# Optimization experiments

Measured on AMD Instinct MI355X. Metric: run time of the kernel, lower is better.

The kernel has to match this reference:

```python
import jax, jax.numpy as jnp
import numpy as np

D = 1024
H = 16
HD = D // H  # 64
FF = 4 * D
EPS = 1e-5


def _xavier(key, shape):
    fan_in, fan_out = shape[1], shape[0]
    limit = float(np.sqrt(6.0 / (fan_in + fan_out)))
    return jax.random.uniform(key, shape, jnp.float32, -limit, limit)


def setup_inputs() -> dict:
    key = jax.random.key(0)
    ks = jax.random.split(key, 8)
    x = jax.random.normal(ks[0], (2, 2048, D), jnp.float32)
    return {
        "x": x,
        "w_qkv": _xavier(ks[1], (3 * D, D)),
        "b_qkv": jnp.zeros((3 * D,), jnp.float32),
        "w_out": _xavier(ks[2], (D, D)),
        "b_out": jnp.zeros((D,), jnp.float32),
        "w1": _xavier(ks[3], (FF, D)),
        "b1": jnp.zeros((FF,), jnp.float32),
        "w2": _xavier(ks[4], (D, FF)),
        "b2": jnp.zeros((D,), jnp.float32),
        "ln1_g": jnp.ones((D,), jnp.float32),
        "ln1_b": jnp.zeros((D,), jnp.float32),
        "ln2_g": jnp.ones((D,), jnp.float32),
        "ln2_b": jnp.zeros((D,), jnp.float32),
    }


def _layernorm(x, g, b):
    mu = jnp.mean(x, -1, keepdims=True)
    var = jnp.mean(jnp.square(x - mu), -1, keepdims=True)
    return (x - mu) * jax.lax.rsqrt(var + EPS) * g + b


def reference(x, w_qkv, b_qkv, w_out, b_out, w1, b1, w2, b2,
              ln1_g, ln1_b, ln2_g, ln2_b):
    B, S, _ = x.shape
    # pre-LN attention branch
    h = _layernorm(x, ln1_g, ln1_b)
    qkv = h @ w_qkv.T + b_qkv                      # [B,S,3D]
    qkv = qkv.reshape(B, S, H, 3 * HD).transpose(0, 2, 1, 3)  # [B,H,S,3hd]
    q, k, v = jnp.split(qkv, 3, axis=-1)
    scores = jnp.einsum('bhqd,bhkd->bhqk', q, k) / np.sqrt(HD)
    attn = jax.nn.softmax(scores, axis=-1)
    ctx = jnp.einsum('bhqk,bhkd->bhqd', attn, v)   # [B,H,S,hd]
    ctx = ctx.transpose(0, 2, 1, 3).reshape(B, S, D)
    x = x + (ctx @ w_out.T + b_out)
    # pre-LN MLP branch
    h = _layernorm(x, ln2_g, ln2_b)
    h = jax.nn.relu(h @ w1.T + b1)
    x = x + (h @ w2.T + b2)
    return x
```

## Files before the change

kernel.cpp:

```cpp
#include <hip/hip_runtime.h>
#include <hip/hip_bf16.h>

typedef __attribute__((ext_vector_type(8))) short bf16x8;
typedef __attribute__((ext_vector_type(4))) float f32x4;
typedef __attribute__((ext_vector_type(16))) float f32x16;
typedef __attribute__((ext_vector_type(4))) unsigned short u16x4;
typedef __attribute__((ext_vector_type(4))) unsigned int u32x4;
typedef unsigned short u16;

__device__ __forceinline__ u16 f2bf(float f) {
  unsigned u = __builtin_bit_cast(unsigned, f);
  u += 0x7fffu + ((u >> 16) & 1u);
  return (u16)(u >> 16);
}
__device__ __forceinline__ float bf2f(u16 u) {
  unsigned v = ((unsigned)u) << 16;
  return __builtin_bit_cast(float, v);
}
__device__ __forceinline__ unsigned cvt_pk_bf16(float lo, float hi) {
  unsigned r;
  asm("v_cvt_pk_bf16_f32 %0, %1, %2" : "=v"(r) : "v"(lo), "v"(hi));
  return r;
}
__device__ __forceinline__ float exp2_fast(float x) {
  float r;
  asm("v_exp_f32 %0, %1" : "=v"(r) : "v"(x));
  return r;
}

__device__ __forceinline__ void gl_lds16(const void* g, void* l) {
  __builtin_amdgcn_global_load_lds((const __attribute__((address_space(1))) void*)g,
                                   (__attribute__((address_space(3))) void*)l,
                                   16, 0, 0);
}

__device__ __forceinline__ void bar() {
  asm volatile("" ::: "memory");
  __builtin_amdgcn_s_barrier();
  asm volatile("" ::: "memory");
}

__global__ __launch_bounds__(256) void cvt_all(const float* __restrict__ a,
                                               const float* __restrict__ b,
                                               const float* __restrict__ c,
                                               const float* __restrict__ d,
                                               u16* __restrict__ oa,
                                               u16* __restrict__ ob,
                                               u16* __restrict__ oc,
                                               u16* __restrict__ od) {
  int i = blockIdx.x * 256 + threadIdx.x;
  const int stride = gridDim.x * 256;
  for (; i < 3145728; i += stride) {
    const float* src;
    u16* dst;
    int j;
    if (i < 786432) { src = a; dst = oa; j = i; }
    else if (i < 1048576) { src = b; dst = ob; j = i - 786432; }
    else if (i < 2097152) { src = c; dst = oc; j = i - 1048576; }
    else { src = d; dst = od; j = i - 2097152; }
    float4 v = ((const float4*)src)[j];
    u16x4 o;
    o.x = f2bf(v.x); o.y = f2bf(v.y); o.z = f2bf(v.z); o.w = f2bf(v.w);
    ((u16x4*)dst)[j] = o;
  }
}

__global__ __launch_bounds__(256) void ln_k(const float* __restrict__ x,
                                            const float* __restrict__ g,
                                            const float* __restrict__ b,
                                            u16* __restrict__ out) {
  const int row = blockIdx.x;
  const int t = threadIdx.x;
  const int lane = t & 63, w = t >> 6;
  const float4 v = ((const float4*)(x + (size_t)row * 1024))[t];
  float s = v.x + v.y + v.z + v.w;
  float q = v.x * v.x + v.y * v.y + v.z * v.z + v.w * v.w;
#pragma unroll
  for (int off = 32; off; off >>= 1) {
    s += __shfl_down(s, off);
    q += __shfl_down(q, off);
  }
  __shared__ float red[8];
  if (lane == 0) { red[w] = s; red[4 + w] = q; }
  __syncthreads();
  s = red[0] + red[1] + red[2] + red[3];
  q = red[4] + red[5] + red[6] + red[7];
  const float mu = s * (1.f / 1024.f);
  const float var = q * (1.f / 1024.f) - mu * mu;
  const float rs = rsqrtf(var + 1e-5f);
  const float4 gv = ((const float4*)g)[t];
  const float4 bv = ((const float4*)b)[t];
  u16x4 o;
  o.x = f2bf((v.x - mu) * rs * gv.x + bv.x);
  o.y = f2bf((v.y - mu) * rs * gv.y + bv.y);
  o.z = f2bf((v.z - mu) * rs * gv.z + bv.z);
  o.w = f2bf((v.w - mu) * rs * gv.w + bv.w);
  ((u16x4*)(out + (size_t)row * 1024))[t] = o;
}

template <int BM, int BN, int TH, int WN, int MR, int NR, int EPI>
__global__ __launch_bounds__(TH, 2) void gemm_rot(const u16* __restrict__ A,
                                                  const u16* __restrict__ B,
                                                  const float* __restrict__ bias,
                                                  const float* __restrict__ res,
                                                  void* __restrict__ outp,
                                                  const int N, const int K) {
  constexpr int AELEMS = BM * 32;
  constexpr int BELEMS = BN * 32;
  constexpr int NC = (BM + BN) * 4 / TH;
  static_assert((BM * 4) % TH == 0 && ((BM + BN) * 4) % TH == 0, "");
  __shared__ u16 lds[3][AELEMS + BELEMS];
  const int t = threadIdx.x;
  const int lane = t & 63, w = t >> 6;
  const int wm = w / WN, wn = w % WN;
  const int l15 = lane & 15, lhi = lane >> 4;
  const int nbx = gridDim.x;
  const int nwg = nbx * gridDim.y;
  const int orig = blockIdx.y * nbx + blockIdx.x;
  const int cpx = nwg >> 3;
  const int lid = (orig & 7) * cpx + (orig >> 3);
  const long bm = (long)(lid / nbx) * BM, bn = (long)(lid % nbx) * BN;
  const u16* Ab = A + bm * K;
  const u16* Bb = B + bn * K;
  const int nk = K >> 5;

#define STAGE(kt_, bufi)                                                      \
  do {                                                                        \
    const long kk_ = (long)(kt_) << 5;                                        \
    _Pragma("unroll")                                                         \
    for (int j = 0; j < NC; ++j) {                                            \
      const int sj = j * TH + t;                                              \
      const u16* src_;                                                        \
      if ((j + 1) * TH <= BM * 4) {                                           \
        src_ = Ab + (size_t)(sj >> 2) * K + kk_ + ((sj & 3) ^ ((sj >> 3) & 3)) * 8; \
      } else {                                                                \
        const int sb_ = sj - BM * 4;                                          \
        src_ = Bb + (size_t)(sb_ >> 2) * K + kk_ + ((sb_ & 3) ^ ((sb_ >> 3) & 3)) * 8; \
      }                                                                       \
      gl_lds16(src_, &lds[bufi][(size_t)(j * TH + w * 64) * 8]);              \
    }                                                                         \
  } while (0)

  f32x4 acc[MR][NR] = {};
  STAGE(0, 0);
  STAGE(1, 1);
  STAGE(2, 2);
  for (int i = 0; i < nk; ++i) {
    if (i + 2 < nk) {
      if constexpr (NC == 4) asm volatile("s_waitcnt vmcnt(8)" ::: "memory");
      else                   asm volatile("s_waitcnt vmcnt(6)" ::: "memory");
    } else if (i + 1 < nk) {
      if constexpr (NC == 4) asm volatile("s_waitcnt vmcnt(4)" ::: "memory");
      else                   asm volatile("s_waitcnt vmcnt(3)" ::: "memory");
    } else {
      asm volatile("s_waitcnt vmcnt(0)" ::: "memory");
    }
    bar();
    const u16* bufA = lds[i % 3];
    const u16* bufB = bufA + AELEMS;
    bf16x8 av[MR], bv[NR];
#pragma unroll
    for (int ii = 0; ii < MR; ++ii) {
      const int R = wm * (MR * 16) + ii * 16 + l15;
      av[ii] = *(const bf16x8*)&bufA[R * 32 + ((lhi ^ ((R >> 1) & 3)) << 3)];
    }
#pragma unroll
    for (int jj = 0; jj < NR; ++jj) {
      const int R = wn * (NR * 16) + jj * 16 + l15;
      bv[jj] = *(const bf16x8*)&bufB[R * 32 + ((lhi ^ ((R >> 1) & 3)) << 3)];
    }
    __builtin_amdgcn_s_setprio(1);
#pragma unroll
    for (int ii = 0; ii < MR; ++ii)
#pragma unroll
      for (int jj = 0; jj < NR; ++jj)
        acc[ii][jj] = __builtin_amdgcn_mfma_f32_16x16x32_bf16(av[ii], bv[jj], acc[ii][jj], 0, 0, 0);
    __builtin_amdgcn_s_setprio(0);
    bar();
    if (i + 3 < nk) STAGE(i + 3, i % 3);
  }
#undef STAGE
#pragma unroll
  for (int jj = 0; jj < NR; ++jj) {
    const long col = bn + wn * (NR * 16) + jj * 16 + l15;
    const float bj = bias[col];
#pragma unroll
    for (int ii = 0; ii < MR; ++ii) {
      const long row0 = bm + wm * (MR * 16) + ii * 16 + lhi * 4;
#pragma unroll
      for (int r = 0; r < 4; ++r) {
        const float v = acc[ii][jj][r] + bj;
        const long idx = (row0 + r) * N + col;
        if constexpr (EPI == 0) {
          ((u16*)outp)[idx] = f2bf(v);
        } else if constexpr (EPI == 1) {
          ((float*)outp)[idx] = v + res[idx];
        } else {
          ((u16*)outp)[idx] = f2bf(v > 0.f ? v : 0.f);
        }
      }
    }
  }
}

__global__ __launch_bounds__(256) void vtrans(const u16* __restrict__ qkv,
                                              u16* __restrict__ vt) {
  const int t = threadIdx.x;
  const int bh = blockIdx.y, b = bh >> 4, h = bh & 15;
  const int kvb = blockIdx.x * 64;
  __shared__ u16 tile[64][72];
  const u16* src = qkv + ((size_t)(b * 2048 + kvb)) * 3072 + h * 192 + 128;
#pragma unroll
  for (int rr = 0; rr < 2; ++rr) {
    const int e = rr * 2048 + t * 8;
    const int kv = e >> 6, d = e & 63;
    *(bf16x8*)&tile[kv][d] = *(const bf16x8*)(src + (size_t)kv * 3072 + d);
  }
  __syncthreads();
#pragma unroll
  for (int rr = 0; rr < 2; ++rr) {
    const int e = rr * 2048 + t * 8;
    const int d = e >> 6, kv = e & 63;
    bf16x8 o;
#pragma unroll
    for (int j = 0; j < 8; ++j) o[j] = (short)tile[kv + j][d];
    *(bf16x8*)(vt + ((size_t)bh * 64 + d) * 2048 + kvb + kv) = o;
  }
}

__global__ __launch_bounds__(256, 4) void attn_k(const u16* __restrict__ qkv,
                                                 const u16* __restrict__ vt,
                                                 u16* __restrict__ part0,
                                                 u16* __restrict__ part1,
                                                 float* __restrict__ ml) {
  __shared__ u16 kt[2][4096];
  __shared__ u16 vtl[2][4096];
  const int t = threadIdx.x;
  const int lane = t & 63, w = t >> 6;
  const int l31 = lane & 31, hl = lane >> 5;
  const int l7 = l31 & 7;
  const int bh = blockIdx.y, b = bh >> 4, h = bh & 15;
  const int qb = blockIdx.x * 128 + w * 32;
  const int sidx = blockIdx.z;
  const int kvbeg = sidx * 1024, kvend = kvbeg + 1024;

  const float qscale = 0.125f * 1.44269504f;
  const u16* qp = qkv + ((size_t)(b * 2048 + qb + l31)) * 3072 + h * 192;
  bf16x8 qf[4];
#pragma unroll
  for (int ds = 0; ds < 4; ++ds) {
    bf16x8 v = *(const bf16x8*)(qp + 16 * ds + 8 * hl);
#pragma unroll
    for (int j = 0; j < 8; ++j) v[j] = (short)f2bf(bf2f((u16)v[j]) * qscale);
    qf[ds] = v;
  }

  const int srow = t >> 3, sgc = t & 7;
  const int sswz = (sgc ^ (srow & 7)) * 8;
  const u16* kg0 = qkv + ((size_t)(b * 2048 + srow)) * 3072 + h * 192 + 64 + sswz;
  const u16* vg0 = vt + (size_t)bh * 64 * 2048 + (size_t)srow * 2048 + sswz;

  f32x16 o0 = {}, o1 = {};
  float m = -1e30f, lsum = 0.f;

#define STAGE(bufi, kv0i)                                              \
  do {                                                                 \
    const u16* ks_ = kg0 + (size_t)(kv0i) * 3072;                      \
    const u16* vs_ = vg0 + (kv0i);                                     \
    gl_lds16(ks_, &kt[bufi][w * 512]);                                 \
    gl_lds16(ks_ + (size_t)32 * 3072, &kt[bufi][2048 + w * 512]);      \
    gl_lds16(vs_, &vtl[bufi][w * 512]);                                \
    gl_lds16(vs_ + (size_t)32 * 2048, &vtl[bufi][2048 + w * 512]);     \
  } while (0)

#define PACK(dst, SA, tl)                                                 \
  do {                                                                    \
    unsigned A0 = cvt_pk_bf16(SA[8 * tl + 0], SA[8 * tl + 1]);            \
    unsigned A1 = cvt_pk_bf16(SA[8 * tl + 2], SA[8 * tl + 3]);            \
    unsigned B0 = cvt_pk_bf16(SA[8 * tl + 4], SA[8 * tl + 5]);            \
    unsigned B1 = cvt_pk_bf16(SA[8 * tl + 6], SA[8 * tl + 7]);            \
    asm volatile("v_permlane32_swap_b32 %0, %1" : "+v"(A0), "+v"(B0));    \
    asm volatile("v_permlane32_swap_b32 %0, %1" : "+v"(A1), "+v"(B1));    \
    u32x4 pv_ = {A0, A1, B0, B1};                                         \
    dst = __builtin_bit_cast(bf16x8, pv_);                                \
  } while (0)

  int buf = 0;
  STAGE(0, kvbeg);
  for (int kv0 = kvbeg; kv0 < kvend; kv0 += 64) {
    if (kv0 + 64 < kvend) {
      STAGE(buf ^ 1, kv0 + 64);
      asm volatile("s_waitcnt vmcnt(4)" ::: "memory");
    } else {
      asm volatile("s_waitcnt vmcnt(0)" ::: "memory");
    }
    bar();
    f32x16 sa0 = {}, sa1 = {};
    __builtin_amdgcn_s_setprio(1);
#pragma unroll
    for (int ds = 0; ds < 4; ++ds) {
      const bf16x8 kf0 = *(const bf16x8*)&kt[buf][l31 * 64 + (((2 * ds + hl) ^ l7) << 3)];
      const bf16x8 kf1 = *(const bf16x8*)&kt[buf][(32 + l31) * 64 + (((2 * ds + hl) ^ l7) << 3)];
      sa0 = __builtin_amdgcn_mfma_f32_32x32x16_bf16(kf0, qf[ds], sa0, 0, 0, 0);
      sa1 = __builtin_amdgcn_mfma_f32_32x32x16_bf16(kf1, qf[ds], sa1, 0, 0, 0);
    }
    __builtin_amdgcn_s_setprio(0);
    float mx[16];
#pragma unroll
    for (int i = 0; i < 16; ++i) mx[i] = fmaxf(sa0[i], sa1[i]);
    const float t0 = fmaxf(fmaxf(mx[0], mx[1]), mx[2]);
    const float t1 = fmaxf(fmaxf(mx[3], mx[4]), mx[5]);
    const float t2 = fmaxf(fmaxf(mx[6], mx[7]), mx[8]);
    const float t3 = fmaxf(fmaxf(mx[9], mx[10]), mx[11]);
    const float t4 = fmaxf(fmaxf(mx[12], mx[13]), mx[14]);
    const float u0 = fmaxf(fmaxf(t0, t1), t2);
    const float u1 = fmaxf(fmaxf(t3, t4), mx[15]);
    float pmax = fmaxf(u0, u1);
    pmax = fmaxf(pmax, __shfl_xor(pmax, 32));
    if (!__all(pmax <= m + 8.f)) {
      const float mn = fmaxf(m, pmax);
      const float sc = exp2_fast(m - mn);
      m = mn;
      lsum *= sc;
      o0 *= sc;
      o1 *= sc;
    }
#pragma unroll
    for (int i = 0; i < 16; ++i) sa0[i] = exp2_fast(sa0[i] - m);
#pragma unroll
    for (int i = 0; i < 16; ++i) sa1[i] = exp2_fast(sa1[i] - m);
    float sm[16];
#pragma unroll
    for (int i = 0; i < 16; ++i) sm[i] = sa0[i] + sa1[i];
#pragma unroll
    for (int st = 8; st; st >>= 1)
#pragma unroll
      for (int i = 0; i < st; ++i) sm[i] += sm[i + st];
    lsum += sm[0] + __shfl_xor(sm[0], 32);
    bf16x8 pf0, pf1, pf2, pf3;
    PACK(pf0, sa0, 0);
    PACK(pf1, sa0, 1);
    PACK(pf2, sa1, 0);
    PACK(pf3, sa1, 1);
    __builtin_amdgcn_s_setprio(1);
#pragma unroll
    for (int t4i = 0; t4i < 4; ++t4i) {
      const bf16x8 vf0 = *(const bf16x8*)&vtl[buf][l31 * 64 + (((2 * t4i + hl) ^ l7) << 3)];
      const bf16x8 vf1 = *(const bf16x8*)&vtl[buf][(32 + l31) * 64 + (((2 * t4i + hl) ^ l7) << 3)];
      const bf16x8 pf = (t4i == 0) ? pf0 : (t4i == 1) ? pf1 : (t4i == 2) ? pf2 : pf3;
      o0 = __builtin_amdgcn_mfma_f32_32x32x16_bf16(vf0, pf, o0, 0, 0, 0);
      o1 = __builtin_amdgcn_mfma_f32_32x32x16_bf16(vf1, pf, o1, 0, 0, 0);
    }
    __builtin_amdgcn_s_setprio(0);
    bar();
    buf ^= 1;
  }
#undef STAGE
#undef PACK
  if (lane < 32) {
    const size_t mi = ((size_t)(sidx * 32 + bh) * 2048 + qb + l31) * 2;
    ml[mi] = m;
    ml[mi + 1] = lsum;
  }
  u16* obase = (sidx == 0) ? part0 : part1;
  u16* ow = ((u16*)kt) + w * 2048;
#pragma unroll
  for (int g2 = 0; g2 < 4; ++g2) {
    uint2 v0, v1;
    v0.x = cvt_pk_bf16(o0[4 * g2 + 0], o0[4 * g2 + 1]);
    v0.y = cvt_pk_bf16(o0[4 * g2 + 2], o0[4 * g2 + 3]);
    v1.x = cvt_pk_bf16(o1[4 * g2 + 0], o1[4 * g2 + 1]);
    v1.y = cvt_pk_bf16(o1[4 * g2 + 2], o1[4 * g2 + 3]);
    *(uint2*)&ow[l31 * 64 + ((g2 ^ l7) << 3) + hl * 4] = v0;
    *(uint2*)&ow[l31 * 64 + (((4 + g2) ^ l7) << 3) + hl * 4] = v1;
  }
#pragma unroll
  for (int p = 0; p < 4; ++p) {
    const int q = 8 * p + (lane >> 3);
    const int gpos = lane & 7;
    const bf16x8 val = *(const bf16x8*)&ow[q * 64 + (gpos << 3)];
    const int gd = gpos ^ (q & 7);
    *(bf16x8*)(obase + ((size_t)(b * 2048 + qb + q)) * 1024 + h * 64 + gd * 8) = val;
  }
}

__global__ __launch_bounds__(256) void attn_merge(const u16* __restrict__ p1,
                                                  const float* __restrict__ ml,
                                                  u16* __restrict__ ctx) {
  const int c = blockIdx.x * 256 + threadIdx.x;
  const int row = c >> 7;
  const int b = row >> 11, q = row & 2047;
  const int h = (c >> 3) & 15;
  const int bh = b * 16 + h;
  const size_t i1 = ((size_t)bh * 2048 + q) * 2;
  const size_t i2 = ((size_t)(32 + bh) * 2048 + q) * 2;
  const float m1 = ml[i1], l1 = ml[i1 + 1];
  const float m2 = ml[i2], l2 = ml[i2 + 1];
  const float M = fmaxf(m1, m2);
  const float w1 = exp2_fast(m1 - M), w2 = exp2_fast(m2 - M);
  const float inv = 1.f / (w1 * l1 + w2 * l2);
  const float a1 = w1 * inv, a2 = w2 * inv;
  const bf16x8 v0 = ((const bf16x8*)ctx)[c];
  const bf16x8 v1 = ((const bf16x8*)p1)[c];
  float r[8];
#pragma unroll
  for (int j = 0; j < 8; ++j)
    r[j] = a1 * bf2f((u16)v0[j]) + a2 * bf2f((u16)v1[j]);
  u32x4 ov = {cvt_pk_bf16(r[0], r[1]), cvt_pk_bf16(r[2], r[3]),
              cvt_pk_bf16(r[4], r[5]), cvt_pk_bf16(r[6], r[7])};
  ((u32x4*)ctx)[c] = ov;
}

extern "C" void kernel_launch(void* const* d_in, const int* in_sizes, int n_in,
                              void* d_out, int out_size, void* d_ws, size_t ws_size,
                              hipStream_t stream) {
  const float* x     = (const float*)d_in[0];
  const float* w_qkv = (const float*)d_in[1];
  const float* b_qkv = (const float*)d_in[2];
  const float* w_out = (const float*)d_in[3];
  const float* b_out = (const float*)d_in[4];
  const float* w1    = (const float*)d_in[5];
  const float* b1    = (const float*)d_in[6];
  const float* w2    = (const float*)d_in[7];
  const float* b2    = (const float*)d_in[8];
  const float* ln1g  = (const float*)d_in[9];
  const float* ln1b  = (const float*)d_in[10];
  const float* ln2g  = (const float*)d_in[11];
  const float* ln2b  = (const float*)d_in[12];
  float* out = (float*)d_out;

  u16* wqkv_b = (u16*)d_ws;
  u16* wout_b = wqkv_b + (size_t)3072 * 1024;
  u16* w1_b   = wout_b + (size_t)1024 * 1024;
  u16* w2_b   = w1_b + (size_t)4096 * 1024;
  u16* r1     = w2_b + (size_t)1024 * 4096;
  u16* r2     = r1 + (size_t)4096 * 1024;
  u16* qkvb   = r2;
  u16* vtb    = r2 + (size_t)4096 * 3072;
  float* x2   = (float*)(r2 + (size_t)4096 * 4096);
  u16* part1  = (u16*)x2;
  float* mlbuf = (float*)(part1 + (size_t)4096 * 1024);

  cvt_all<<<2048, 256, 0, stream>>>(w_qkv, w_out, w1, w2,
                                    wqkv_b, wout_b, w1_b, w2_b);

  ln_k<<<4096, 256, 0, stream>>>(x, ln1g, ln1b, r1);
  gemm_rot<128, 128, 256, 2, 4, 4, 0><<<dim3(24, 32), 256, 0, stream>>>(
      r1, wqkv_b, b_qkv, nullptr, qkvb, 3072, 1024);
  vtrans<<<dim3(32, 32), 256, 0, stream>>>(qkvb, vtb);
  attn_k<<<dim3(16, 32, 2), 256, 0, stream>>>(qkvb, vtb, r1, part1, mlbuf);
  attn_merge<<<2048, 256, 0, stream>>>(part1, mlbuf, r1);
  gemm_rot<64, 128, 256, 2, 2, 4, 1><<<dim3(8, 64), 256, 0, stream>>>(
      r1, wout_b, b_out, x, x2, 1024, 1024);
  ln_k<<<4096, 256, 0, stream>>>(x2, ln2g, ln2b, r1);
  gemm_rot<128, 128, 256, 2, 4, 4, 2><<<dim3(32, 32), 256, 0, stream>>>(
      r1, w1_b, b1, nullptr, r2, 4096, 1024);
  gemm_rot<64, 128, 256, 2, 2, 4, 1><<<dim3(8, 64), 256, 0, stream>>>(
      r2, w2_b, b2, x2, out, 1024, 4096);
}
```

Before: 247.5 us.

## Add BK template parameter with XOR swizzle; enlarge QKV/FFN1 tiles to 128x256

Generalises the GEMM to a configurable K-tile depth, adding a row&7 XOR swizzle for 64-wide K tiles and multiple MFMA k-substeps per LDS stage. The out-projection and FFN2 GEMMs now use BK=64, which halves the number of barrier/wait iterations. The QKV and FFN1 GEMMs move to 128x256 tiles with 512 threads, giving more reuse per block at the cost of fewer blocks and more LDS per block. Larger LDS footprints may cut occupancy, and the grid is now 384 or 512 blocks where it was 768 or 1024.

```diff
diff --git a/kernel.cpp b/kernel.cpp
--- a/kernel.cpp
+++ b/kernel.cpp
@@ -98,17 +98,19 @@
   ((u16x4*)(out + (size_t)row * 1024))[t] = o;
 }
 
-template <int BM, int BN, int TH, int WN, int MR, int NR, int EPI>
+template <int BM, int BN, int BK, int TH, int WN, int MR, int NR, int EPI>
 __global__ __launch_bounds__(TH, 2) void gemm_rot(const u16* __restrict__ A,
                                                   const u16* __restrict__ B,
                                                   const float* __restrict__ bias,
                                                   const float* __restrict__ res,
                                                   void* __restrict__ outp,
                                                   const int N, const int K) {
-  constexpr int AELEMS = BM * 32;
-  constexpr int BELEMS = BN * 32;
-  constexpr int NC = (BM + BN) * 4 / TH;
-  static_assert((BM * 4) % TH == 0 && ((BM + BN) * 4) % TH == 0, "");
+  constexpr int GPR = BK / 8;
+  constexpr int KS = BK / 32;
+  constexpr int AELEMS = BM * BK;
+  constexpr int BELEMS = BN * BK;
+  constexpr int NC = (BM + BN) * GPR / TH;
+  static_assert((BM * GPR) % TH == 0 && ((BM + BN) * GPR) % TH == 0, "");
   __shared__ u16 lds[3][AELEMS + BELEMS];
   const int t = threadIdx.x;
   const int lane = t & 63, w = t >> 6;
@@ -122,20 +124,26 @@
   const long bm = (long)(lid / nbx) * BM, bn = (long)(lid % nbx) * BN;
   const u16* Ab = A + bm * K;
   const u16* Bb = B + bn * K;
-  const int nk = K >> 5;
+  const int nk = K / BK;
 
 #define STAGE(kt_, bufi)                                                      \
   do {                                                                        \
-    const long kk_ = (long)(kt_) << 5;                                        \
+    const long kk_ = (long)(kt_) * BK;                                        \
     _Pragma("unroll")                                                         \
     for (int j = 0; j < NC; ++j) {                                            \
       const int sj = j * TH + t;                                              \
       const u16* src_;                                                        \
-      if ((j + 1) * TH <= BM * 4) {                                           \
-        src_ = Ab + (size_t)(sj >> 2) * K + kk_ + ((sj & 3) ^ ((sj >> 3) & 3)) * 8; \
+      if ((j + 1) * TH <= BM * GPR) {                                         \
+        const int row_ = sj / GPR, grp_ = sj % GPR;                           \
+        const int g_ = (BK == 32) ? (grp_ ^ ((row_ >> 1) & 3))                \
+                                  : (grp_ ^ (row_ & 7));                      \
+        src_ = Ab + (size_t)row_ * K + kk_ + g_ * 8;                          \
       } else {                                                                \
-        const int sb_ = sj - BM * 4;                                          \
-        src_ = Bb + (size_t)(sb_ >> 2) * K + kk_ + ((sb_ & 3) ^ ((sb_ >> 3) & 3)) * 8; \
+        const int sb_ = sj - BM * GPR;                                        \
+        const int row_ = sb_ / GPR, grp_ = sb_ % GPR;                         \
+        const int g_ = (BK == 32) ? (grp_ ^ ((row_ >> 1) & 3))                \
+                                  : (grp_ ^ (row_ & 7));                      \
+        src_ = Bb + (size_t)row_ * K + kk_ + g_ * 8;                          \
       }                                                                       \
       gl_lds16(src_, &lds[bufi][(size_t)(j * TH + w * 64) * 8]);              \
     }                                                                         \
@@ -147,34 +155,49 @@
   STAGE(2, 2);
   for (int i = 0; i < nk; ++i) {
     if (i + 2 < nk) {
-      if constexpr (NC == 4) asm volatile("s_waitcnt vmcnt(8)" ::: "memory");
-      else                   asm volatile("s_waitcnt vmcnt(6)" ::: "memory");
+      if constexpr (NC == 3)      asm volatile("s_waitcnt vmcnt(6)" ::: "memory");
+      else if constexpr (NC == 4) asm volatile("s_waitcnt vmcnt(8)" ::: "memory");
+      else                        asm volatile("s_waitcnt vmcnt(12)" ::: "memory");
     } else if (i + 1 < nk) {
-      if constexpr (NC == 4) asm volatile("s_waitcnt vmcnt(4)" ::: "memory");
-      else                   asm volatile("s_waitcnt vmcnt(3)" ::: "memory");
+      if constexpr (NC == 3)      asm volatile("s_waitcnt vmcnt(3)" ::: "memory");
+      else if constexpr (NC == 4) asm volatile("s_waitcnt vmcnt(4)" ::: "memory");
+      else                        asm volatile("s_waitcnt vmcnt(6)" ::: "memory");
     } else {
       asm volatile("s_waitcnt vmcnt(0)" ::: "memory");
     }
     bar();
     const u16* bufA = lds[i % 3];
     const u16* bufB = bufA + AELEMS;
-    bf16x8 av[MR], bv[NR];
+    bf16x8 av[MR][KS], bv[NR][KS];
 #pragma unroll
     for (int ii = 0; ii < MR; ++ii) {
       const int R = wm * (MR * 16) + ii * 16 + l15;
-      av[ii] = *(const bf16x8*)&bufA[R * 32 + ((lhi ^ ((R >> 1) & 3)) << 3)];
+#pragma unroll
+      for (int ks = 0; ks < KS; ++ks) {
+        const int pos = (BK == 32) ? (lhi ^ ((R >> 1) & 3))
+                                   : ((ks * 4 + lhi) ^ (R & 7));
+        av[ii][ks] = *(const bf16x8*)&bufA[R * BK + (pos << 3)];
+      }
     }
 #pragma unroll
     for (int jj = 0; jj < NR; ++jj) {
       const int R = wn * (NR * 16) + jj * 16 + l15;
-      bv[jj] = *(const bf16x8*)&bufB[R * 32 + ((lhi ^ ((R >> 1) & 3)) << 3)];
+#pragma unroll
+      for (int ks = 0; ks < KS; ++ks) {
+        const int pos = (BK == 32) ? (lhi ^ ((R >> 1) & 3))
+                                   : ((ks * 4 + lhi) ^ (R & 7));
+        bv[jj][ks] = *(const bf16x8*)&bufB[R * BK + (pos << 3)];
+      }
     }
     __builtin_amdgcn_s_setprio(1);
 #pragma unroll
     for (int ii = 0; ii < MR; ++ii)
 #pragma unroll
       for (int jj = 0; jj < NR; ++jj)
-        acc[ii][jj] = __builtin_amdgcn_mfma_f32_16x16x32_bf16(av[ii], bv[jj], acc[ii][jj], 0, 0, 0);
+#pragma unroll
+        for (int ks = 0; ks < KS; ++ks)
+          acc[ii][jj] = __builtin_amdgcn_mfma_f32_16x16x32_bf16(av[ii][ks], bv[jj][ks],
+                                                                acc[ii][jj], 0, 0, 0);
     __builtin_amdgcn_s_setprio(0);
     bar();
     if (i + 3 < nk) STAGE(i + 3, i % 3);
@@ -445,16 +468,16 @@
                                     wqkv_b, wout_b, w1_b, w2_b);
 
   ln_k<<<4096, 256, 0, stream>>>(x, ln1g, ln1b, r1);
-  gemm_rot<128, 128, 256, 2, 4, 4, 0><<<dim3(24, 32), 256, 0, stream>>>(
+  gemm_rot<128, 256, 32, 512, 4, 4, 4, 0><<<dim3(12, 32), 512, 0, stream>>>(
       r1, wqkv_b, b_qkv, nullptr, qkvb, 3072, 1024);
   vtrans<<<dim3(32, 32), 256, 0, stream>>>(qkvb, vtb);
   attn_k<<<dim3(16, 32, 2), 256, 0, stream>>>(qkvb, vtb, r1, part1, mlbuf);
   attn_merge<<<2048, 256, 0, stream>>>(part1, mlbuf, r1);
-  gemm_rot<64, 128, 256, 2, 2, 4, 1><<<dim3(8, 64), 256, 0, stream>>>(
+  gemm_rot<64, 128, 64, 256, 2, 2, 4, 1><<<dim3(8, 64), 256, 0, stream>>>(
       r1, wout_b, b_out, x, x2, 1024, 1024);
   ln_k<<<4096, 256, 0, stream>>>(x2, ln2g, ln2b, r1);
-  gemm_rot<128, 128, 256, 2, 4, 4, 2><<<dim3(32, 32), 256, 0, stream>>>(
+  gemm_rot<128, 256, 32, 512, 4, 4, 4, 2><<<dim3(16, 32), 512, 0, stream>>>(
       r1, w1_b, b1, nullptr, r2, 4096, 1024);
-  gemm_rot<64, 128, 256, 2, 2, 4, 1><<<dim3(8, 64), 256, 0, stream>>>(
+  gemm_rot<64, 128, 64, 256, 2, 2, 4, 1><<<dim3(8, 64), 256, 0, stream>>>(
       r2, w2_b, b2, x2, out, 1024, 4096);
 }
```

Measured after the change: 220.2 us. -11.1%, faster.
